# Kernel tuning notes

Hardware: AMD Instinct MI355X
Metric: run time of the kernel (lower is better)

The kernel has to match this reference:

```python
import jax, jax.numpy as jnp
import numpy as np

B, QL, HID = 4, 1, 4096
H, KVH, D = 16, 4, 256      # num_heads, num_kv_heads, head_dim
PAST = 8191
S = PAST + QL               # kv_seq_len = 8192
K_KEEP, R = 2048, 128       # heavy-hitter budget, channel top-r
THETA = 10000.0


def _rotate_half(x):
    return jnp.concatenate([-x[..., D // 2:], x[..., :D // 2]], axis=-1)


def _rope_tables(seq_len):
    inv_freq = 1.0 / (THETA ** (jnp.arange(0, D, 2, dtype=jnp.float32) / D))
    t = jnp.arange(seq_len, dtype=jnp.float32)
    freqs = jnp.outer(t, inv_freq)
    emb = jnp.concatenate([freqs, freqs], axis=-1)  # [S, D]
    return jnp.cos(emb), jnp.sin(emb)


def setup_inputs() -> dict:
    key = jax.random.key(0)
    ks = jax.random.split(key, 8)
    w = 0.02
    return {
        "hidden_states": jax.random.normal(ks[0], (B, QL, HID), jnp.float32),
        "attention_mask": jnp.zeros((B, 1, QL, S), jnp.float32),
        "position_ids": jnp.full((B, QL), PAST, jnp.int32),
        "past_key": jax.random.normal(ks[1], (B, KVH, PAST, D), jnp.float32),
        "past_value": jax.random.normal(ks[2], (B, KVH, PAST, D), jnp.float32),
        "Wq": w * jax.random.normal(ks[3], (H * D, HID), jnp.float32),
        "Wk": w * jax.random.normal(ks[4], (KVH * D, HID), jnp.float32),
        "Wv": w * jax.random.normal(ks[5], (KVH * D, HID), jnp.float32),
        "Wo": w * jax.random.normal(ks[6], (HID, H * D), jnp.float32),
    }


def reference(hidden_states, attention_mask, position_ids, past_key, past_value, Wq, Wk, Wv, Wo):
    b, q_len, _ = hidden_states.shape
    # QKV projections (no bias)
    q = (hidden_states @ Wq.T).reshape(b, q_len, H, D).transpose(0, 2, 1, 3)    # [b,H,q,D]
    k = (hidden_states @ Wk.T).reshape(b, q_len, KVH, D).transpose(0, 2, 1, 3)  # [b,KVH,q,D]
    v = (hidden_states @ Wv.T).reshape(b, q_len, KVH, D).transpose(0, 2, 1, 3)

    # RoPE at the current positions
    cos_t, sin_t = _rope_tables(S)
    cos = cos_t[position_ids][:, None]  # [b,1,q,D]
    sin = sin_t[position_ids][:, None]
    q = q * cos + _rotate_half(q) * sin
    k = k * cos + _rotate_half(k) * sin

    # append to KV cache, then GQA repeat (repeat_interleave over head dim)
    key = jnp.concatenate([past_key, k], axis=2)      # [b,KVH,S,D]
    value = jnp.concatenate([past_value, v], axis=2)
    n_rep = H // KVH
    key_r = jnp.repeat(key, n_rep, axis=1)            # [b,H,S,D]
    value_r = jnp.repeat(value, n_rep, axis=1)

    # --- heavy-hitter approximate scores: top-r channels of |q| ---
    i1 = jax.lax.top_k(jnp.abs(q), R)[1]                                   # [b,H,q,R]
    Q_hat = jnp.take_along_axis(q, i1, axis=-1)                            # [b,H,q,R]
    K_hat = jnp.take_along_axis(key_r, jnp.broadcast_to(i1, (b, H, S, R)), axis=-1)  # [b,H,S,R]
    scale = jnp.sqrt(D * jnp.abs(Q_hat).sum(-1, keepdims=True)
                     / jnp.abs(q).sum(-1, keepdims=True))                  # [b,H,q,1]
    s_hat = jax.nn.softmax(jnp.einsum('bhqr,bhsr->bhqs', Q_hat, K_hat) / scale
                           + attention_mask, axis=-1)                      # [b,H,q,S]

    # --- evict all but the top-k heavy hitters (rank of s_hat, descending) ---
    ranks = jnp.argsort(jnp.argsort(-s_hat, axis=-1), axis=-1)             # [b,H,q,S]
    aw = jnp.einsum('bhqd,bhsd->bhqs', q, key_r) / np.sqrt(D).astype(np.float32)
    aw = jnp.where(ranks >= K_KEEP, -jnp.inf, aw) + attention_mask
    probs = jax.nn.softmax(aw, axis=-1)
    y = jnp.einsum('bhqs,bhsd->bhqd', probs, value_r)                      # [b,H,q,D]

    out = y.transpose(0, 2, 1, 3).reshape(b, q_len, H * D) @ Wo.T          # [b,q,HID]
    return out
```

## Files before the change

kernel.cpp:

```cpp
#include <hip/hip_runtime.h>
#include <cmath>

#define B_   4
#define H_   16
#define KVH_ 4
#define D_   256
#define HID_ 4096
#define PAST_ 8191
#define S_   8192
#define KKEEP_ 2048
#define R_   128

#define OFF_Q     0
#define OFF_KN    16384
#define OFF_VN    20480
#define OFF_SCALE 24576
#define OFF_CMASK 24640
#define OFF_F     32768
#define OFF_A     557056
#define OFF_P     1081344
#define OFF_YP    1605632
#define OFF_Y     2129920

__global__ __launch_bounds__(256) void k1_qkv(
    const float* __restrict__ hidden, const int* __restrict__ pos_ids,
    const float* __restrict__ Wq, const float* __restrict__ Wk, const float* __restrict__ Wv,
    float* __restrict__ q_ws, float* __restrict__ knew, float* __restrict__ vnew)
{
    int slot = blockIdx.x >> 7;
    int d    = blockIdx.x & 127;
    const float* W; float* outp; int head; bool rope; int bstride;
    if (slot < 16)      { W = Wq; head = slot;      outp = q_ws + head * D_; rope = true;  bstride = H_ * D_; }
    else if (slot < 20) { W = Wk; head = slot - 16; outp = knew + head * D_; rope = true;  bstride = KVH_ * D_; }
    else                { W = Wv; head = slot - 20; outp = vnew + head * D_; rope = false; bstride = KVH_ * D_; }

    int rowbase = head * D_ + d;
    const float* w0 = W + (size_t)rowbase * HID_;
    const float* w1 = W + (size_t)(rowbase + 128) * HID_;

    float acc0[4] = {0.f, 0.f, 0.f, 0.f};
    float acc1[4] = {0.f, 0.f, 0.f, 0.f};
#pragma unroll
    for (int i = 0; i < 4; ++i) {
        int c = (threadIdx.x + 256 * i) * 4;
        float4 a0 = *(const float4*)(w0 + c);
        float4 a1 = *(const float4*)(w1 + c);
#pragma unroll
        for (int b = 0; b < 4; ++b) {
            float4 hv = *(const float4*)(hidden + b * HID_ + c);
            acc0[b] += a0.x * hv.x + a0.y * hv.y + a0.z * hv.z + a0.w * hv.w;
            acc1[b] += a1.x * hv.x + a1.y * hv.y + a1.z * hv.z + a1.w * hv.w;
        }
    }
#pragma unroll
    for (int off = 1; off < 64; off <<= 1) {
#pragma unroll
        for (int b = 0; b < 4; ++b) {
            acc0[b] += __shfl_xor(acc0[b], off, 64);
            acc1[b] += __shfl_xor(acc1[b], off, 64);
        }
    }
    __shared__ float red[4][8];
    int wv = threadIdx.x >> 6, ln = threadIdx.x & 63;
    if (ln == 0) {
#pragma unroll
        for (int b = 0; b < 4; ++b) { red[wv][b] = acc0[b]; red[wv][4 + b] = acc1[b]; }
    }
    __syncthreads();
    if (threadIdx.x == 0) {
        float x = (float)d * (1.0f / 128.0f);
        float invf = 1.0f / powf(10000.0f, x);
        for (int b = 0; b < 4; ++b) {
            float s0 = red[0][b] + red[1][b] + red[2][b] + red[3][b];
            float s1 = red[0][4 + b] + red[1][4 + b] + red[2][4 + b] + red[3][4 + b];
            float o0, o1;
            if (rope) {
                float ang = (float)pos_ids[b] * invf;
                double ad = (double)ang;
                float c = (float)cos(ad), sn = (float)sin(ad);
                o0 = s0 * c - s1 * sn;
                o1 = s1 * c + s0 * sn;
            } else { o0 = s0; o1 = s1; }
            outp[b * bstride + d]       = o0;
            outp[b * bstride + d + 128] = o1;
        }
    }
}

__global__ __launch_bounds__(256) void k1b_chan(
    const float* __restrict__ q_ws, float* __restrict__ scale_ws, unsigned* __restrict__ cmask_ws)
{
    int bh = blockIdx.x;
    int t  = threadIdx.x;
    __shared__ unsigned ua[256];
    __shared__ float red[256];
    __shared__ unsigned bm[8];
    __shared__ float s_all;

    float qv = q_ws[bh * 256 + t];
    float aq = fabsf(qv);
    ua[t] = __float_as_uint(aq);
    if (t < 8) bm[t] = 0u;
    __syncthreads();

    unsigned mine = ua[t];
    int rank = 0;
    for (int i = 0; i < 256; ++i) {
        unsigned o = ua[i];
        rank += (o > mine) || (o == mine && i < t);
    }
    bool kept = rank < R_;
    if (kept) atomicOr(&bm[t >> 5], 1u << (t & 31));

    red[t] = aq; __syncthreads();
    for (int off = 128; off; off >>= 1) { if (t < off) red[t] += red[t + off]; __syncthreads(); }
    if (t == 0) s_all = red[0];
    __syncthreads();
    red[t] = kept ? aq : 0.f; __syncthreads();
    for (int off = 128; off; off >>= 1) { if (t < off) red[t] += red[t + off]; __syncthreads(); }
    if (t == 0) scale_ws[bh] = sqrtf(256.0f * red[0] / s_all);
    if (t < 8) cmask_ws[bh * 8 + t] = bm[t];
}

__global__ __launch_bounds__(256) void k2_scores(
    const float* __restrict__ past_key, const float* __restrict__ knew,
    const float* __restrict__ q_ws, const float* __restrict__ scale_ws,
    const unsigned* __restrict__ cmask_ws, const float* __restrict__ amask,
    float* __restrict__ fsc, float* __restrict__ asc)
{
    int bkv   = blockIdx.x >> 6;
    int chunk = blockIdx.x & 63;
    int b = bkv >> 2, kvh = bkv & 3;
    int w = threadIdx.x >> 6, lane = threadIdx.x & 63;
    int g = lane >> 4, m = lane & 15;
    int h = kvh * 4 + g;

    const float* qp = q_ws + (b * H_ + h) * D_;
    const unsigned* cm = cmask_ws + (b * H_ + h) * 8;
    float inv_scale = 1.0f / scale_ws[b * H_ + h];

    float qr[16], ar[16];
#pragma unroll
    for (int i = 0; i < 4; ++i)
#pragma unroll
        for (int t = 0; t < 4; ++t) {
            int c = i * 64 + m * 4 + t;
            float q = qp[c];
            qr[i * 4 + t] = q;
            ar[i * 4 + t] = ((cm[c >> 5] >> (c & 31)) & 1u) ? q : 0.f;
        }

    const float* kbase = past_key + (size_t)(b * KVH_ + kvh) * PAST_ * D_;
    const float* knrow = knew + (b * KVH_ + kvh) * D_;
    float* fout = fsc + (size_t)(b * H_ + h) * S_;
    float* aout = asc + (size_t)(b * H_ + h) * S_;
    const float* mrow = amask + b * S_;
    int s0 = chunk * 128 + w;

    const float* r0 = (s0 < PAST_) ? (kbase + (size_t)s0 * D_) : knrow;
    float4 n0 = *(const float4*)(r0 + m * 4);
    float4 n1 = *(const float4*)(r0 + 64 + m * 4);
    float4 n2 = *(const float4*)(r0 + 128 + m * 4);
    float4 n3 = *(const float4*)(r0 + 192 + m * 4);

    for (int it = 0; it < 32; ++it) {
        int s = s0 + it * 4;
        float4 c0 = n0, c1 = n1, c2 = n2, c3 = n3;
        if (it < 31) {
            int sn = s + 4;
            const float* rn = (sn < PAST_) ? (kbase + (size_t)sn * D_) : knrow;
            n0 = *(const float4*)(rn + m * 4);
            n1 = *(const float4*)(rn + 64 + m * 4);
            n2 = *(const float4*)(rn + 128 + m * 4);
            n3 = *(const float4*)(rn + 192 + m * 4);
        }
        float full = 0.f, appr = 0.f;
        full += qr[0]*c0.x + qr[1]*c0.y + qr[2]*c0.z + qr[3]*c0.w;
        appr += ar[0]*c0.x + ar[1]*c0.y + ar[2]*c0.z + ar[3]*c0.w;
        full += qr[4]*c1.x + qr[5]*c1.y + qr[6]*c1.z + qr[7]*c1.w;
        appr += ar[4]*c1.x + ar[5]*c1.y + ar[6]*c1.z + ar[7]*c1.w;
        full += qr[8]*c2.x + qr[9]*c2.y + qr[10]*c2.z + qr[11]*c2.w;
        appr += ar[8]*c2.x + ar[9]*c2.y + ar[10]*c2.z + ar[11]*c2.w;
        full += qr[12]*c3.x + qr[13]*c3.y + qr[14]*c3.z + qr[15]*c3.w;
        appr += ar[12]*c3.x + ar[13]*c3.y + ar[14]*c3.z + ar[15]*c3.w;
#pragma unroll
        for (int off = 1; off < 16; off <<= 1) {
            full += __shfl_xor(full, off, 64);
            appr += __shfl_xor(appr, off, 64);
        }
        if (m == 0)      fout[s] = full * 0.0625f + mrow[s];
        else if (m == 1) aout[s] = appr * inv_scale + mrow[s];
    }
}

#define PAD(s) ((s) + ((s) >> 5))
__global__ __launch_bounds__(1024) void k3_select(
    const float* __restrict__ fsc, const float* __restrict__ asc, float* __restrict__ probs)
{
    int bh = blockIdx.x;
    int t  = threadIdx.x;
    int lane = t & 63, wid = t >> 6;
    __shared__ unsigned ua[8448];
    __shared__ unsigned hist2[16 * 257];
    __shared__ unsigned hist[256];
    __shared__ unsigned sf[256];
    __shared__ int wsum[16], wbase[16];
    __shared__ float wred[16];
    __shared__ unsigned sh_bin; __shared__ int sh_rem;
    __shared__ float sh_M, sh_Z;

    const float* ap = asc + (size_t)bh * S_;
    const float* fp = fsc + (size_t)bh * S_;

#pragma unroll
    for (int i = 0; i < 8; ++i) {
        int s = i * 1024 + t;
        unsigned u = __float_as_uint(ap[s]);
        u ^= (u & 0x80000000u) ? 0xFFFFFFFFu : 0x80000000u;
        ua[PAD(s)] = u;
    }

    unsigned prefix = 0; int rem = KKEEP_;
    for (int pass = 0; pass < 4; ++pass) {
        const int shift = 24 - 8 * pass;
        for (int j = t; j < 16 * 257; j += 1024) hist2[j] = 0;
        __syncthreads();
#pragma unroll
        for (int i = 0; i < 8; ++i) {
            unsigned u = ua[PAD(i * 1024 + t)];
            bool match = (pass == 0) || ((u >> (shift + 8)) == prefix);
            if (match) atomicAdd(&hist2[wid * 257 + ((u >> shift) & 255u)], 1u);
        }
        __syncthreads();
        if (t < 256) {
            unsigned hsum = 0;
#pragma unroll
            for (int w2 = 0; w2 < 16; ++w2) hsum += hist2[w2 * 257 + t];
            hist[t] = hsum;
        }
        __syncthreads();
        if (t < 64) {
            unsigned h0 = hist[t*4], h1 = hist[t*4+1], h2 = hist[t*4+2], h3 = hist[t*4+3];
            unsigned loc = h0 + h1 + h2 + h3;
            unsigned run = loc;
#pragma unroll
            for (int off = 1; off < 64; off <<= 1) {
                unsigned v = __shfl_down(run, off, 64);
                if (t + off < 64) run += v;
            }
            unsigned tail = run - loc;
            sf[t*4+3] = tail + h3;
            sf[t*4+2] = tail + h3 + h2;
            sf[t*4+1] = tail + h3 + h2 + h1;
            sf[t*4+0] = tail + loc;
        }
        __syncthreads();
        if (t < 256) {
            unsigned above = (t == 255) ? 0u : sf[t + 1];
            if (sf[t] >= (unsigned)rem && above < (unsigned)rem) {
                sh_bin = (unsigned)t;
                sh_rem = rem - (int)above;
            }
        }
        __syncthreads();
        prefix = (prefix << 8) | sh_bin;
        rem = sh_rem;
        __syncthreads();
    }
    unsigned ut = prefix; int Need = rem;

    int cnt = 0;
#pragma unroll
    for (int i = 0; i < 8; ++i)
        cnt += (ua[PAD(t * 8 + i)] == ut) ? 1 : 0;
    int inc = cnt;
#pragma unroll
    for (int off = 1; off < 64; off <<= 1) {
        int v = __shfl_up(inc, off, 64);
        if (lane >= off) inc += v;
    }
    if (lane == 63) wsum[wid] = inc;
    __syncthreads();
    if (t == 0) {
        int run = 0;
#pragma unroll
        for (int j = 0; j < 16; ++j) { int c = wsum[j]; wbase[j] = run; run += c; }
    }
    __syncthreads();
    int eqb = wbase[wid] + inc - cnt;
#pragma unroll
    for (int i = 0; i < 8; ++i) {
        int s = t * 8 + i;
        if (ua[PAD(s)] == ut) {
            ua[PAD(s)] = (eqb < Need) ? 0xFFFFFFFFu : 0u;
            ++eqb;
        }
    }
    __syncthreads();

    float m = -3.4e38f, z = 0.f;
#pragma unroll
    for (int i = 0; i < 8; ++i) {
        int s = i * 1024 + t;
        if (ua[PAD(s)] > ut) {
            float f = fp[s];
            if (f > m) { z = z * expf(m - f) + 1.f; m = f; }
            else       { z += expf(f - m); }
        }
    }
    float wm = m;
#pragma unroll
    for (int off = 1; off < 64; off <<= 1) wm = fmaxf(wm, __shfl_xor(wm, off, 64));
    if (lane == 0) wred[wid] = wm;
    __syncthreads();
    if (t == 0) {
        float M = wred[0];
#pragma unroll
        for (int j = 1; j < 16; ++j) M = fmaxf(M, wred[j]);
        sh_M = M;
    }
    __syncthreads();
    float M = sh_M;
    float zs = z * expf(m - M);
#pragma unroll
    for (int off = 1; off < 64; off <<= 1) zs += __shfl_xor(zs, off, 64);
    if (lane == 0) wred[wid] = zs;
    __syncthreads();
    if (t == 0) {
        float Z = 0.f;
#pragma unroll
        for (int j = 0; j < 16; ++j) Z += wred[j];
        sh_Z = Z;
    }
    __syncthreads();
    float invZ = 1.0f / sh_Z;

    float* pp = probs + (size_t)bh * S_;
#pragma unroll
    for (int i = 0; i < 8; ++i) {
        int s = i * 1024 + t;
        pp[s] = (ua[PAD(s)] > ut) ? expf(fp[s] - M) * invZ : 0.f;
    }
}

__global__ __launch_bounds__(256) void k4_wv(
    const float* __restrict__ past_value, const float* __restrict__ vnew,
    const float* __restrict__ probs, float* __restrict__ ypart)
{
    const int NCH = 32;
    int bkv = blockIdx.x / NCH, chunk = blockIdx.x - bkv * NCH;
    int b = bkv >> 2, kvh = bkv & 3;
    int w = threadIdx.x >> 6, lane = threadIdx.x & 63;
    int h0 = kvh * 4;

    const float* p0 = probs + (size_t)(b * H_ + h0) * S_;
    const float* vbase = past_value + (size_t)(b * KVH_ + kvh) * PAST_ * D_;
    const float* vnrow = vnew + (b * KVH_ + kvh) * D_;

    float acc[4][4] = {{0.f}};
    int s0 = chunk * 256 + w;

    const float* vr0 = (s0 < PAST_) ? (vbase + (size_t)s0 * D_) : vnrow;
    float4 vn = *(const float4*)(vr0 + lane * 4);
    float pn0 = p0[s0], pn1 = p0[S_ + s0], pn2 = p0[2 * S_ + s0], pn3 = p0[3 * S_ + s0];

    for (int it = 0; it < 64; ++it) {
        float4 vc = vn;
        float c0 = pn0, c1 = pn1, c2 = pn2, c3 = pn3;
        if (it < 63) {
            int sn = s0 + it * 4 + 4;
            const float* vrn = (sn < PAST_) ? (vbase + (size_t)sn * D_) : vnrow;
            vn = *(const float4*)(vrn + lane * 4);
            pn0 = p0[sn]; pn1 = p0[S_ + sn]; pn2 = p0[2 * S_ + sn]; pn3 = p0[3 * S_ + sn];
        }
        acc[0][0] += c0 * vc.x; acc[0][1] += c0 * vc.y; acc[0][2] += c0 * vc.z; acc[0][3] += c0 * vc.w;
        acc[1][0] += c1 * vc.x; acc[1][1] += c1 * vc.y; acc[1][2] += c1 * vc.z; acc[1][3] += c1 * vc.w;
        acc[2][0] += c2 * vc.x; acc[2][1] += c2 * vc.y; acc[2][2] += c2 * vc.z; acc[2][3] += c2 * vc.w;
        acc[3][0] += c3 * vc.x; acc[3][1] += c3 * vc.y; acc[3][2] += c3 * vc.z; acc[3][3] += c3 * vc.w;
    }

    __shared__ float part[4][4][256];
#pragma unroll
    for (int j = 0; j < 4; ++j)
#pragma unroll
        for (int t4 = 0; t4 < 4; ++t4)
            part[w][j][lane * 4 + t4] = acc[j][t4];
    __syncthreads();

    float* yo = ypart + (size_t)(chunk * 16 + bkv) * 1024;
    for (int o = threadIdx.x; o < 1024; o += 256) {
        int j = o >> 8, d = o & 255;
        yo[o] = part[0][j][d] + part[1][j][d] + part[2][j][d] + part[3][j][d];
    }
}

__global__ __launch_bounds__(256) void k5_reduce(const float* __restrict__ ypart, float* __restrict__ yflat)
{
    int bh = blockIdx.x; int b = bh >> 4, h = bh & 15;
    int kvh = h >> 2, j = h & 3;
    int d = threadIdx.x;
    int bkv = b * 4 + kvh;
    float sum = 0.f;
    for (int c = 0; c < 32; ++c)
        sum += ypart[(size_t)(c * 16 + bkv) * 1024 + j * 256 + d];
    yflat[b * 4096 + h * 256 + d] = sum;
}

__global__ __launch_bounds__(256) void k6_out(
    const float* __restrict__ Wo, const float* __restrict__ yflat, float* __restrict__ out)
{
    int i = blockIdx.x;
    const float* wrow = Wo + (size_t)i * HID_;
    float acc[4] = {0.f, 0.f, 0.f, 0.f};
#pragma unroll
    for (int ii = 0; ii < 4; ++ii) {
        int c = (threadIdx.x + 256 * ii) * 4;
        float4 wv = *(const float4*)(wrow + c);
#pragma unroll
        for (int b = 0; b < 4; ++b) {
            float4 yv = *(const float4*)(yflat + b * 4096 + c);
            acc[b] += wv.x * yv.x + wv.y * yv.y + wv.z * yv.z + wv.w * yv.w;
        }
    }
#pragma unroll
    for (int off = 1; off < 64; off <<= 1)
#pragma unroll
        for (int b = 0; b < 4; ++b) acc[b] += __shfl_xor(acc[b], off, 64);
    __shared__ float red[4][4];
    int wv_ = threadIdx.x >> 6, ln = threadIdx.x & 63;
    if (ln == 0)
#pragma unroll
        for (int b = 0; b < 4; ++b) red[wv_][b] = acc[b];
    __syncthreads();
    if (threadIdx.x < 4) {
        int b = threadIdx.x;
        out[b * HID_ + i] = red[0][b] + red[1][b] + red[2][b] + red[3][b];
    }
}

extern "C" void kernel_launch(void* const* d_in, const int* in_sizes, int n_in,
                              void* d_out, int out_size, void* d_ws, size_t ws_size,
                              hipStream_t stream)
{
    const float* hidden = (const float*)d_in[0];
    const float* amask  = (const float*)d_in[1];
    const int*   posids = (const int*)d_in[2];
    const float* pkey   = (const float*)d_in[3];
    const float* pval   = (const float*)d_in[4];
    const float* Wq     = (const float*)d_in[5];
    const float* Wk     = (const float*)d_in[6];
    const float* Wv     = (const float*)d_in[7];
    const float* Wo     = (const float*)d_in[8];
    float* out = (float*)d_out;
    float* ws  = (float*)d_ws;

    float* q_ws   = ws + OFF_Q;
    float* knew   = ws + OFF_KN;
    float* vnew   = ws + OFF_VN;
    float* scale  = ws + OFF_SCALE;
    unsigned* cmask = (unsigned*)(ws + OFF_CMASK);
    float* fsc    = ws + OFF_F;
    float* asc    = ws + OFF_A;
    float* probs  = ws + OFF_P;
    float* ypart  = ws + OFF_YP;
    float* yflat  = ws + OFF_Y;

    k1_qkv  <<<dim3(3072), dim3(256), 0, stream>>>(hidden, posids, Wq, Wk, Wv, q_ws, knew, vnew);
    k1b_chan<<<dim3(64),   dim3(256), 0, stream>>>(q_ws, scale, cmask);
    k2_scores<<<dim3(1024), dim3(256), 0, stream>>>(pkey, knew, q_ws, scale, cmask, amask, fsc, asc);
    k3_select<<<dim3(64),  dim3(1024), 0, stream>>>(fsc, asc, probs);
    k4_wv   <<<dim3(512),  dim3(256), 0, stream>>>(pval, vnew, probs, ypart);
    k5_reduce<<<dim3(64),  dim3(256), 0, stream>>>(ypart, yflat);
    k6_out  <<<dim3(4096), dim3(256), 0, stream>>>(Wo, yflat, out);
}
```

Before: 444.9 us.

## Double grid size and process two contiguous rows per wave in score and PV kernels

The score kernel and the weighted-value kernel each launch twice as many blocks. Each wave now walks a contiguous run of key/value rows two at a time instead of striding by four, which gives more independent loads in flight and lets the mask, probability and output accesses be vectorised as float2. The partial-sum buffer doubles to 64 chunks, so the reduce kernel loops over 64 partials and the yflat offset moves to make room. The cost is more partial-sum traffic and more registers per thread.

```diff
diff --git a/kernel.cpp b/kernel.cpp
--- a/kernel.cpp
+++ b/kernel.cpp
@@ -20,7 +20,7 @@
 #define OFF_A     557056
 #define OFF_P     1081344
 #define OFF_YP    1605632
-#define OFF_Y     2129920
+#define OFF_Y     2654208
 
 __global__ __launch_bounds__(256) void k1_qkv(
     const float* __restrict__ hidden, const int* __restrict__ pos_ids,
@@ -128,8 +128,8 @@
     const unsigned* __restrict__ cmask_ws, const float* __restrict__ amask,
     float* __restrict__ fsc, float* __restrict__ asc)
 {
-    int bkv   = blockIdx.x >> 6;
-    int chunk = blockIdx.x & 63;
+    int bkv   = blockIdx.x >> 7;
+    int chunk = blockIdx.x & 127;
     int b = bkv >> 2, kvh = bkv & 3;
     int w = threadIdx.x >> 6, lane = threadIdx.x & 63;
     int g = lane >> 4, m = lane & 15;
@@ -155,41 +155,68 @@
     float* fout = fsc + (size_t)(b * H_ + h) * S_;
     float* aout = asc + (size_t)(b * H_ + h) * S_;
     const float* mrow = amask + b * S_;
-    int s0 = chunk * 128 + w;
-
-    const float* r0 = (s0 < PAST_) ? (kbase + (size_t)s0 * D_) : knrow;
-    float4 n0 = *(const float4*)(r0 + m * 4);
-    float4 n1 = *(const float4*)(r0 + 64 + m * 4);
-    float4 n2 = *(const float4*)(r0 + 128 + m * 4);
-    float4 n3 = *(const float4*)(r0 + 192 + m * 4);
-
-    for (int it = 0; it < 32; ++it) {
-        int s = s0 + it * 4;
-        float4 c0 = n0, c1 = n1, c2 = n2, c3 = n3;
-        if (it < 31) {
-            int sn = s + 4;
-            const float* rn = (sn < PAST_) ? (kbase + (size_t)sn * D_) : knrow;
-            n0 = *(const float4*)(rn + m * 4);
-            n1 = *(const float4*)(rn + 64 + m * 4);
-            n2 = *(const float4*)(rn + 128 + m * 4);
-            n3 = *(const float4*)(rn + 192 + m * 4);
-        }
-        float full = 0.f, appr = 0.f;
-        full += qr[0]*c0.x + qr[1]*c0.y + qr[2]*c0.z + qr[3]*c0.w;
-        appr += ar[0]*c0.x + ar[1]*c0.y + ar[2]*c0.z + ar[3]*c0.w;
-        full += qr[4]*c1.x + qr[5]*c1.y + qr[6]*c1.z + qr[7]*c1.w;
-        appr += ar[4]*c1.x + ar[5]*c1.y + ar[6]*c1.z + ar[7]*c1.w;
-        full += qr[8]*c2.x + qr[9]*c2.y + qr[10]*c2.z + qr[11]*c2.w;
-        appr += ar[8]*c2.x + ar[9]*c2.y + ar[10]*c2.z + ar[11]*c2.w;
-        full += qr[12]*c3.x + qr[13]*c3.y + qr[14]*c3.z + qr[15]*c3.w;
-        appr += ar[12]*c3.x + ar[13]*c3.y + ar[14]*c3.z + ar[15]*c3.w;
+    int s0 = chunk * 64 + w * 16;
+
+    const float* rA = (s0     < PAST_) ? (kbase + (size_t)s0 * D_)       : knrow;
+    const float* rB = (s0 + 1 < PAST_) ? (kbase + (size_t)(s0 + 1) * D_) : knrow;
+    float4 nA0 = *(const float4*)(rA + m * 4);
+    float4 nA1 = *(const float4*)(rA + 64 + m * 4);
+    float4 nA2 = *(const float4*)(rA + 128 + m * 4);
+    float4 nA3 = *(const float4*)(rA + 192 + m * 4);
+    float4 nB0 = *(const float4*)(rB + m * 4);
+    float4 nB1 = *(const float4*)(rB + 64 + m * 4);
+    float4 nB2 = *(const float4*)(rB + 128 + m * 4);
+    float4 nB3 = *(const float4*)(rB + 192 + m * 4);
+
+    for (int it = 0; it < 8; ++it) {
+        int sA = s0 + 2 * it;
+        float4 cA0 = nA0, cA1 = nA1, cA2 = nA2, cA3 = nA3;
+        float4 cB0 = nB0, cB1 = nB1, cB2 = nB2, cB3 = nB3;
+        if (it < 7) {
+            int sn = sA + 2;
+            const float* pA = (sn     < PAST_) ? (kbase + (size_t)sn * D_)       : knrow;
+            const float* pB = (sn + 1 < PAST_) ? (kbase + (size_t)(sn + 1) * D_) : knrow;
+            nA0 = *(const float4*)(pA + m * 4);
+            nA1 = *(const float4*)(pA + 64 + m * 4);
+            nA2 = *(const float4*)(pA + 128 + m * 4);
+            nA3 = *(const float4*)(pA + 192 + m * 4);
+            nB0 = *(const float4*)(pB + m * 4);
+            nB1 = *(const float4*)(pB + 64 + m * 4);
+            nB2 = *(const float4*)(pB + 128 + m * 4);
+            nB3 = *(const float4*)(pB + 192 + m * 4);
+        }
+        float fullA = 0.f, apprA = 0.f, fullB = 0.f, apprB = 0.f;
+        fullA += qr[0]*cA0.x + qr[1]*cA0.y + qr[2]*cA0.z + qr[3]*cA0.w;
+        apprA += ar[0]*cA0.x + ar[1]*cA0.y + ar[2]*cA0.z + ar[3]*cA0.w;
+        fullA += qr[4]*cA1.x + qr[5]*cA1.y + qr[6]*cA1.z + qr[7]*cA1.w;
+        apprA += ar[4]*cA1.x + ar[5]*cA1.y + ar[6]*cA1.z + ar[7]*cA1.w;
+        fullA += qr[8]*cA2.x + qr[9]*cA2.y + qr[10]*cA2.z + qr[11]*cA2.w;
+        apprA += ar[8]*cA2.x + ar[9]*cA2.y + ar[10]*cA2.z + ar[11]*cA2.w;
+        fullA += qr[12]*cA3.x + qr[13]*cA3.y + qr[14]*cA3.z + qr[15]*cA3.w;
+        apprA += ar[12]*cA3.x + ar[13]*cA3.y + ar[14]*cA3.z + ar[15]*cA3.w;
+        fullB += qr[0]*cB0.x + qr[1]*cB0.y + qr[2]*cB0.z + qr[3]*cB0.w;
+        apprB += ar[0]*cB0.x + ar[1]*cB0.y + ar[2]*cB0.z + ar[3]*cB0.w;
+        fullB += qr[4]*cB1.x + qr[5]*cB1.y + qr[6]*cB1.z + qr[7]*cB1.w;
+        apprB += ar[4]*cB1.x + ar[5]*cB1.y + ar[6]*cB1.z + ar[7]*cB1.w;
+        fullB += qr[8]*cB2.x + qr[9]*cB2.y + qr[10]*cB2.z + qr[11]*cB2.w;
+        apprB += ar[8]*cB2.x + ar[9]*cB2.y + ar[10]*cB2.z + ar[11]*cB2.w;
+        fullB += qr[12]*cB3.x + qr[13]*cB3.y + qr[14]*cB3.z + qr[15]*cB3.w;
+        apprB += ar[12]*cB3.x + ar[13]*cB3.y + ar[14]*cB3.z + ar[15]*cB3.w;
 #pragma unroll
         for (int off = 1; off < 16; off <<= 1) {
-            full += __shfl_xor(full, off, 64);
-            appr += __shfl_xor(appr, off, 64);
-        }
-        if (m == 0)      fout[s] = full * 0.0625f + mrow[s];
-        else if (m == 1) aout[s] = appr * inv_scale + mrow[s];
+            fullA += __shfl_xor(fullA, off, 64);
+            apprA += __shfl_xor(apprA, off, 64);
+            fullB += __shfl_xor(fullB, off, 64);
+            apprB += __shfl_xor(apprB, off, 64);
+        }
+        float2 mv = *(const float2*)(mrow + sA);
+        if (m == 0) {
+            float2 o; o.x = fullA * 0.0625f + mv.x; o.y = fullB * 0.0625f + mv.y;
+            *(float2*)(fout + sA) = o;
+        } else if (m == 1) {
+            float2 o; o.x = apprA * inv_scale + mv.x; o.y = apprB * inv_scale + mv.y;
+            *(float2*)(aout + sA) = o;
+        }
     }
 }
 
@@ -347,8 +374,7 @@
     const float* __restrict__ past_value, const float* __restrict__ vnew,
     const float* __restrict__ probs, float* __restrict__ ypart)
 {
-    const int NCH = 32;
-    int bkv = blockIdx.x / NCH, chunk = blockIdx.x - bkv * NCH;
+    int bkv = blockIdx.x >> 6, chunk = blockIdx.x & 63;
     int b = bkv >> 2, kvh = bkv & 3;
     int w = threadIdx.x >> 6, lane = threadIdx.x & 63;
     int h0 = kvh * 4;
@@ -358,25 +384,47 @@
     const float* vnrow = vnew + (b * KVH_ + kvh) * D_;
 
     float acc[4][4] = {{0.f}};
-    int s0 = chunk * 256 + w;
-
-    const float* vr0 = (s0 < PAST_) ? (vbase + (size_t)s0 * D_) : vnrow;
-    float4 vn = *(const float4*)(vr0 + lane * 4);
-    float pn0 = p0[s0], pn1 = p0[S_ + s0], pn2 = p0[2 * S_ + s0], pn3 = p0[3 * S_ + s0];
-
-    for (int it = 0; it < 64; ++it) {
-        float4 vc = vn;
-        float c0 = pn0, c1 = pn1, c2 = pn2, c3 = pn3;
-        if (it < 63) {
-            int sn = s0 + it * 4 + 4;
-            const float* vrn = (sn < PAST_) ? (vbase + (size_t)sn * D_) : vnrow;
-            vn = *(const float4*)(vrn + lane * 4);
-            pn0 = p0[sn]; pn1 = p0[S_ + sn]; pn2 = p0[2 * S_ + sn]; pn3 = p0[3 * S_ + sn];
-        }
-        acc[0][0] += c0 * vc.x; acc[0][1] += c0 * vc.y; acc[0][2] += c0 * vc.z; acc[0][3] += c0 * vc.w;
-        acc[1][0] += c1 * vc.x; acc[1][1] += c1 * vc.y; acc[1][2] += c1 * vc.z; acc[1][3] += c1 * vc.w;
-        acc[2][0] += c2 * vc.x; acc[2][1] += c2 * vc.y; acc[2][2] += c2 * vc.z; acc[2][3] += c2 * vc.w;
-        acc[3][0] += c3 * vc.x; acc[3][1] += c3 * vc.y; acc[3][2] += c3 * vc.z; acc[3][3] += c3 * vc.w;
+    int s0 = chunk * 128 + w * 32;
+
+    const float* rA = (s0     < PAST_) ? (vbase + (size_t)s0 * D_)       : vnrow;
+    const float* rB = (s0 + 1 < PAST_) ? (vbase + (size_t)(s0 + 1) * D_) : vnrow;
+    float4 vnA = *(const float4*)(rA + lane * 4);
+    float4 vnB = *(const float4*)(rB + lane * 4);
+    float2 pn0 = *(const float2*)(p0 + s0);
+    float2 pn1 = *(const float2*)(p0 + S_ + s0);
+    float2 pn2 = *(const float2*)(p0 + 2 * S_ + s0);
+    float2 pn3 = *(const float2*)(p0 + 3 * S_ + s0);
+
+    for (int it = 0; it < 16; ++it) {
+        float4 vA = vnA, vB = vnB;
+        float2 c0 = pn0, c1 = pn1, c2 = pn2, c3 = pn3;
+        if (it < 15) {
+            int sn = s0 + 2 * it + 2;
+            const float* pA = (sn     < PAST_) ? (vbase + (size_t)sn * D_)       : vnrow;
+            const float* pB = (sn + 1 < PAST_) ? (vbase + (size_t)(sn + 1) * D_) : vnrow;
+            vnA = *(const float4*)(pA + lane * 4);
+            vnB = *(const float4*)(pB + lane * 4);
+            pn0 = *(const float2*)(p0 + sn);
+            pn1 = *(const float2*)(p0 + S_ + sn);
+            pn2 = *(const float2*)(p0 + 2 * S_ + sn);
+            pn3 = *(const float2*)(p0 + 3 * S_ + sn);
+        }
+        acc[0][0] += c0.x * vA.x + c0.y * vB.x;
+        acc[0][1] += c0.x * vA.y + c0.y * vB.y;
+        acc[0][2] += c0.x * vA.z + c0.y * vB.z;
+        acc[0][3] += c0.x * vA.w + c0.y * vB.w;
+        acc[1][0] += c1.x * vA.x + c1.y * vB.x;
+        acc[1][1] += c1.x * vA.y + c1.y * vB.y;
+        acc[1][2] += c1.x * vA.z + c1.y * vB.z;
+        acc[1][3] += c1.x * vA.w + c1.y * vB.w;
+        acc[2][0] += c2.x * vA.x + c2.y * vB.x;
+        acc[2][1] += c2.x * vA.y + c2.y * vB.y;
+        acc[2][2] += c2.x * vA.z + c2.y * vB.z;
+        acc[2][3] += c2.x * vA.w + c2.y * vB.w;
+        acc[3][0] += c3.x * vA.x + c3.y * vB.x;
+        acc[3][1] += c3.x * vA.y + c3.y * vB.y;
+        acc[3][2] += c3.x * vA.z + c3.y * vB.z;
+        acc[3][3] += c3.x * vA.w + c3.y * vB.w;
     }
 
     __shared__ float part[4][4][256];
@@ -401,7 +449,7 @@
     int d = threadIdx.x;
     int bkv = b * 4 + kvh;
     float sum = 0.f;
-    for (int c = 0; c < 32; ++c)
+    for (int c = 0; c < 64; ++c)
         sum += ypart[(size_t)(c * 16 + bkv) * 1024 + j * 256 + d];
     yflat[b * 4096 + h * 256 + d] = sum;
 }
@@ -467,9 +515,9 @@
 
     k1_qkv  <<<dim3(3072), dim3(256), 0, stream>>>(hidden, posids, Wq, Wk, Wv, q_ws, knew, vnew);
     k1b_chan<<<dim3(64),   dim3(256), 0, stream>>>(q_ws, scale, cmask);
-    k2_scores<<<dim3(1024), dim3(256), 0, stream>>>(pkey, knew, q_ws, scale, cmask, amask, fsc, asc);
+    k2_scores<<<dim3(2048), dim3(256), 0, stream>>>(pkey, knew, q_ws, scale, cmask, amask, fsc, asc);
     k3_select<<<dim3(64),  dim3(1024), 0, stream>>>(fsc, asc, probs);
-    k4_wv   <<<dim3(512),  dim3(256), 0, stream>>>(pval, vnew, probs, ypart);
+    k4_wv   <<<dim3(1024), dim3(256), 0, stream>>>(pval, vnew, probs, ypart);
     k5_reduce<<<dim3(64),  dim3(256), 0, stream>>>(ypart, yflat);
     k6_out  <<<dim3(4096), dim3(256), 0, stream>>>(Wo, yflat, out);
 }
```

Result: faster. 425.6 us (-4.3%).
